# Performance work log

Hardware: AMD Instinct MI355X
Metric: run time of the kernel (lower is better)

Reference implementation:

```python
import jax, jax.numpy as jnp
import numpy as np

N_NODES = 100000

def gcn_conv(x, W, b, src, dst, norm, num_nodes):
    # Linear transform first (PyG GCNConv), then normalized scatter-add over edges.
    h = x @ W  # [N, d_out]
    msgs = norm[:, None] * h[src]  # gather source features, scale by sym norm
    out = jax.ops.segment_sum(msgs, dst, num_segments=num_nodes)
    return out + b

def gcn_norm(edge_index, num_nodes):
    # add self loops, compute deg^-1/2[src] * deg^-1/2[dst] per edge (PyG gcn_norm)
    loops = jnp.arange(num_nodes, dtype=edge_index.dtype)
    src = jnp.concatenate([edge_index[0], loops])
    dst = jnp.concatenate([edge_index[1], loops])
    deg = jax.ops.segment_sum(jnp.ones_like(dst, dtype=jnp.float32), dst, num_segments=num_nodes)
    dinv = jnp.where(deg > 0, jax.lax.rsqrt(deg), 0.0)
    norm = dinv[src] * dinv[dst]
    return src, dst, norm

def setup_inputs() -> dict:
    key = jax.random.key(0)
    k1, k2, k3, k4 = jax.random.split(key, 4)
    x = jax.random.normal(k1, (N_NODES, 512), dtype=jnp.float32)
    edge_index = jax.random.randint(k2, (2, 1600000), 0, N_NODES, dtype=jnp.int32)
    W1 = jax.random.normal(k3, (512, 128), dtype=jnp.float32) * (1.0 / np.sqrt(512))
    b1 = jnp.zeros((128,), dtype=jnp.float32)
    W2 = jax.random.normal(k4, (128, 40), dtype=jnp.float32) * (1.0 / np.sqrt(128))
    b2 = jnp.zeros((40,), dtype=jnp.float32)
    return {"x": x, "edge_index": edge_index, "W1": W1, "b1": b1, "W2": W2, "b2": b2}

def reference(x, edge_index, W1, b1, W2, b2):
    src, dst, norm = gcn_norm(edge_index, N_NODES)
    h = jax.nn.relu(gcn_conv(x, W1, b1, src, dst, norm, N_NODES))
    # dropout is identity in eval mode
    logits = gcn_conv(h, W2, b2, src, dst, norm, N_NODES)
    return jax.nn.log_softmax(logits, axis=1)
```

## Files before the change

### kernel.cpp

```cpp
#include <hip/hip_runtime.h>
#include <hip/hip_bf16.h>
#include <math.h>

typedef __attribute__((ext_vector_type(8))) short short8v;
typedef __attribute__((ext_vector_type(4))) unsigned short ushort4v;
typedef __attribute__((ext_vector_type(8))) unsigned short ushort8v;
typedef __attribute__((ext_vector_type(4))) unsigned uint4v;
typedef __attribute__((ext_vector_type(4))) float f32x4;

__device__ inline unsigned short f2bf(float f) {
    unsigned u = __float_as_uint(f);
    return (unsigned short)((u + 0x7fffu + ((u >> 16) & 1u)) >> 16);
}
__device__ inline float bflo(unsigned u) { return __uint_as_float(u << 16); }
__device__ inline float bfhi(unsigned u) { return __uint_as_float(u & 0xffff0000u); }
__device__ inline float bf1(unsigned short s) { return __uint_as_float((unsigned)s << 16); }
__device__ inline unsigned pk2(float a, float b) {
    __hip_bfloat162 h = __float22bfloat162_rn(make_float2(a, b));
    unsigned r;
    __builtin_memcpy(&r, &h, 4);
    return r;
}

__global__ void k_deg(const int* __restrict__ dst, int* __restrict__ deg,
                      int* __restrict__ rank, int E) {
    int e = blockIdx.x * blockDim.x + threadIdx.x;
    if (e < E) rank[e] = atomicAdd(&deg[dst[e]], 1);
}

__global__ __launch_bounds__(256) void k_bsum(const int* __restrict__ deg,
                                              int* __restrict__ bsum, int n) {
    __shared__ int r[256];
    int b = blockIdx.x, tid = threadIdx.x;
    int i0 = b * 1024 + tid * 4;
    int s = 0;
#pragma unroll
    for (int j = 0; j < 4; ++j)
        if (i0 + j < n) s += deg[i0 + j];
    r[tid] = s;
    __syncthreads();
    for (int off = 128; off > 0; off >>= 1) {
        if (tid < off) r[tid] += r[tid + off];
        __syncthreads();
    }
    if (tid == 0) bsum[b] = r[0];
}

__global__ __launch_bounds__(1024) void k_scan2(const int* __restrict__ bsum,
                                                int* __restrict__ bpre,
                                                int* __restrict__ total_out, int nb) {
    __shared__ int ls[1024];
    int tid = threadIdx.x;
    int v = (tid < nb) ? bsum[tid] : 0;
    ls[tid] = v;
    __syncthreads();
    for (int off = 1; off < 1024; off <<= 1) {
        int t = (tid >= off) ? ls[tid - off] : 0;
        __syncthreads();
        ls[tid] += t;
        __syncthreads();
    }
    if (tid < nb) bpre[tid] = ls[tid] - v;
    if (tid == 1023) *total_out = ls[1023];
}

__global__ __launch_bounds__(256) void k_scan3(const int* __restrict__ deg,
                                               const int* __restrict__ bpre,
                                               int* __restrict__ offsets,
                                               float* __restrict__ dinv, int n) {
    __shared__ int ts[256];
    int b = blockIdx.x, tid = threadIdx.x;
    int i0 = b * 1024 + tid * 4;
    int v[4] = {0, 0, 0, 0};
#pragma unroll
    for (int j = 0; j < 4; ++j)
        if (i0 + j < n) v[j] = deg[i0 + j];
    int s = v[0] + v[1] + v[2] + v[3];
    ts[tid] = s;
    __syncthreads();
    for (int off = 1; off < 256; off <<= 1) {
        int t = (tid >= off) ? ts[tid - off] : 0;
        __syncthreads();
        ts[tid] += t;
        __syncthreads();
    }
    int excl = bpre[b] + ts[tid] - s;
#pragma unroll
    for (int j = 0; j < 4; ++j) {
        if (i0 + j < n) {
            offsets[i0 + j] = excl;
            dinv[i0 + j] = rsqrtf((float)(v[j] + 1));
        }
        excl += v[j];
    }
}

__global__ void k_fill(const int* __restrict__ src, const int* __restrict__ dst,
                       const int* __restrict__ offsets, const int* __restrict__ rank,
                       int* __restrict__ esrc, int E) {
    int e = blockIdx.x * blockDim.x + threadIdx.x;
    if (e < E) esrc[offsets[dst[e]] + rank[e]] = src[e];
}

__global__ void k_wswz(const float* __restrict__ W1, unsigned short* __restrict__ Wswz) {
    int t = blockIdx.x * blockDim.x + threadIdx.x;
    if (t >= 16 * 8 * 64) return;
    int l = t & 63, cb = (t >> 6) & 7, ks = t >> 9;
    int col = cb * 16 + (l & 15);
    int kb = ks * 32 + 8 * (l >> 4);
    ushort8v w;
#pragma unroll
    for (int j = 0; j < 8; ++j) w[j] = f2bf(W1[(size_t)(kb + j) * 128 + col]);
    *(ushort8v*)(Wswz + (size_t)t * 8) = w;
}

#define AP 40
#define CP 132

__global__ __launch_bounds__(256) void k_gemm1(const float* __restrict__ x,
                                               const unsigned short* __restrict__ Wswz,
                                               const float* __restrict__ dinv,
                                               unsigned short* __restrict__ h0s, int M) {
    __shared__ __align__(16) unsigned short lds[64 * CP];
    int tid = threadIdx.x;
    int wc = tid >> 6, lane = tid & 63;
    int g = lane >> 4, lr = lane & 15;
    int brow = blockIdx.x * 64;

    int srow = tid >> 2, sq = tid & 3;
    int sgr = brow + srow;
    const float* xp = (sgr < M) ? (x + (size_t)sgr * 512 + sq * 8) : nullptr;

    f32x4 acc[4][2];
#pragma unroll
    for (int m = 0; m < 4; ++m)
#pragma unroll
        for (int n = 0; n < 2; ++n) acc[m][n] = (f32x4){0.f, 0.f, 0.f, 0.f};

    float4 paA = make_float4(0.f, 0.f, 0.f, 0.f), pbA = paA;
    float4 paB = paA, pbB = paA;
    if (xp) {
        paA = *(const float4*)xp;          pbA = *(const float4*)(xp + 4);
        paB = *(const float4*)(xp + 32);   pbB = *(const float4*)(xp + 36);
    }

#pragma unroll 1
    for (int ks = 0; ks < 16; ks += 2) {
        {
            unsigned short* As = lds;
            union { uint4v u; short8v s; } cv;
            cv.u[0] = pk2(paA.x, paA.y); cv.u[1] = pk2(paA.z, paA.w);
            cv.u[2] = pk2(pbA.x, pbA.y); cv.u[3] = pk2(pbA.z, pbA.w);
            *(short8v*)&As[srow * AP + sq * 8] = cv.s;
            __syncthreads();
            if (ks + 2 < 16 && xp) {
                const float* np = xp + (ks + 2) * 32;
                paA = *(const float4*)np; pbA = *(const float4*)(np + 4);
            }
            short8v bfr[2];
#pragma unroll
            for (int n = 0; n < 2; ++n) {
                int cb = wc * 2 + n;
                bfr[n] = *(const short8v*)(Wswz + (size_t)((ks * 8 + cb) * 64 + lane) * 8);
            }
            short8v afr[4];
#pragma unroll
            for (int m = 0; m < 4; ++m)
                afr[m] = *(const short8v*)&As[(m * 16 + lr) * AP + g * 8];
#pragma unroll
            for (int m = 0; m < 4; ++m)
#pragma unroll
                for (int n = 0; n < 2; ++n)
                    acc[m][n] = __builtin_amdgcn_mfma_f32_16x16x32_bf16(afr[m], bfr[n],
                                                                        acc[m][n], 0, 0, 0);
        }
        {
            unsigned short* As = lds + 2560;
            union { uint4v u; short8v s; } cv;
            cv.u[0] = pk2(paB.x, paB.y); cv.u[1] = pk2(paB.z, paB.w);
            cv.u[2] = pk2(pbB.x, pbB.y); cv.u[3] = pk2(pbB.z, pbB.w);
            *(short8v*)&As[srow * AP + sq * 8] = cv.s;
            __syncthreads();
            if (ks + 3 < 16 && xp) {
                const float* np = xp + (ks + 3) * 32;
                paB = *(const float4*)np; pbB = *(const float4*)(np + 4);
            }
            int k1 = ks + 1;
            short8v bfr[2];
#pragma unroll
            for (int n = 0; n < 2; ++n) {
                int cb = wc * 2 + n;
                bfr[n] = *(const short8v*)(Wswz + (size_t)((k1 * 8 + cb) * 64 + lane) * 8);
            }
            short8v afr[4];
#pragma unroll
            for (int m = 0; m < 4; ++m)
                afr[m] = *(const short8v*)&As[(m * 16 + lr) * AP + g * 8];
#pragma unroll
            for (int m = 0; m < 4; ++m)
#pragma unroll
                for (int n = 0; n < 2; ++n)
                    acc[m][n] = __builtin_amdgcn_mfma_f32_16x16x32_bf16(afr[m], bfr[n],
                                                                        acc[m][n], 0, 0, 0);
        }
    }
    __syncthreads();
#pragma unroll
    for (int m = 0; m < 4; ++m) {
        int row0 = m * 16 + g * 4;
        float dv[4];
#pragma unroll
        for (int r = 0; r < 4; ++r) {
            int gr = brow + row0 + r;
            dv[r] = (gr < M) ? dinv[gr] : 0.f;
        }
#pragma unroll
        for (int n = 0; n < 2; ++n) {
            int col = wc * 32 + n * 16 + lr;
#pragma unroll
            for (int r = 0; r < 4; ++r)
                lds[(row0 + r) * CP + col] = f2bf(acc[m][n][r] * dv[r]);
        }
    }
    __syncthreads();
    if (sgr < M) {
        unsigned short* dst = h0s + (size_t)sgr * 128;
        const unsigned short* src = &lds[srow * CP];
#pragma unroll
        for (int i = 0; i < 4; ++i) {
            int c = i * 32 + sq * 8;
            *(ushort4v*)(dst + c)     = *(const ushort4v*)(src + c);
            *(ushort4v*)(dst + c + 4) = *(const ushort4v*)(src + c + 4);
        }
    }
}

__global__ __launch_bounds__(256) void k_agg1(const unsigned short* __restrict__ h0s,
                                              const float* __restrict__ dinv,
                                              const int* __restrict__ offsets,
                                              const int* __restrict__ esrc,
                                              const float* __restrict__ b1,
                                              unsigned* __restrict__ h1b, int N) {
    int wid = (blockIdx.x * 256 + threadIdx.x) >> 6;
    if (wid >= N) return;
    int lane = threadIdx.x & 63;
    int half = lane >> 5, hl = lane & 31;
    const uint2* base = (const uint2*)h0s;
    uint2 us = base[(size_t)wid * 32 + hl];
    float ax0, ay0, ax1, ay1;
    if (half == 0) {
        ax0 = bflo(us.x); ay0 = bfhi(us.x); ax1 = bflo(us.y); ay1 = bfhi(us.y);
    } else {
        ax0 = ay0 = ax1 = ay1 = 0.f;
    }
    int beg = offsets[wid], end = offsets[wid + 1];
    for (int b0 = beg; b0 < end; b0 += 64) {
        int nb = min(64, end - b0);
        int idx = (lane < nb) ? esrc[b0 + lane] : 0;
        int k = 0;
        for (; k + 32 <= nb; k += 32) {
            uint2 v[16];
#pragma unroll
            for (int j = 0; j < 16; ++j) {
                int s = __shfl(idx, k + 2 * j + half);
                v[j] = base[(size_t)s * 32 + hl];
            }
#pragma unroll
            for (int j = 0; j < 16; ++j) {
                ax0 += bflo(v[j].x); ay0 += bfhi(v[j].x);
                ax1 += bflo(v[j].y); ay1 += bfhi(v[j].y);
            }
        }
        for (; k + 8 <= nb; k += 8) {
            uint2 v[4];
#pragma unroll
            for (int j = 0; j < 4; ++j) {
                int s = __shfl(idx, k + 2 * j + half);
                v[j] = base[(size_t)s * 32 + hl];
            }
#pragma unroll
            for (int j = 0; j < 4; ++j) {
                ax0 += bflo(v[j].x); ay0 += bfhi(v[j].x);
                ax1 += bflo(v[j].y); ay1 += bfhi(v[j].y);
            }
        }
        for (; k + 2 <= nb; k += 2) {
            int s = __shfl(idx, k + half);
            uint2 v = base[(size_t)s * 32 + hl];
            ax0 += bflo(v.x); ay0 += bfhi(v.x);
            ax1 += bflo(v.y); ay1 += bfhi(v.y);
        }
        if (k < nb) {
            int s = __shfl(idx, k);
            uint2 v = base[(size_t)s * 32 + hl];
            if (half == 0) {
                ax0 += bflo(v.x); ay0 += bfhi(v.x);
                ax1 += bflo(v.y); ay1 += bfhi(v.y);
            }
        }
    }
    ax0 += __shfl_xor(ax0, 32); ay0 += __shfl_xor(ay0, 32);
    ax1 += __shfl_xor(ax1, 32); ay1 += __shfl_xor(ay1, 32);
    if (half == 0) {
        float di = dinv[wid];
        float4 bb = ((const float4*)b1)[hl];
        float r0 = fmaxf(fmaf(di, ax0, bb.x), 0.f);
        float r1 = fmaxf(fmaf(di, ay0, bb.y), 0.f);
        float r2 = fmaxf(fmaf(di, ax1, bb.z), 0.f);
        float r3 = fmaxf(fmaf(di, ay1, bb.w), 0.f);
        uint2 o;
        o.x = pk2(r0, r1);
        o.y = pk2(r2, r3);
        ((uint2*)h1b)[(size_t)wid * 32 + hl] = o;
    }
}

__global__ __launch_bounds__(256) void k_gemm2(const unsigned* __restrict__ h1b,
                                               const float* __restrict__ W2,
                                               const float* __restrict__ dinv,
                                               unsigned short* __restrict__ h2s, int N) {
    __shared__ float w2s[128 * 40];
    int tid = threadIdx.x;
    for (int i = tid; i < 128 * 40; i += 256) w2s[i] = W2[i];
    __syncthreads();
    int r = blockIdx.x * 256 + tid;
    if (r >= N) return;
    const uint4v* row = (const uint4v*)(h1b + (size_t)r * 64);
    float acc[40];
#pragma unroll
    for (int c = 0; c < 40; ++c) acc[c] = 0.f;
    for (int c8 = 0; c8 < 16; ++c8) {
        uint4v u = row[c8];
        float aa[8];
#pragma unroll
        for (int j = 0; j < 4; ++j) {
            aa[2 * j]     = bflo(u[j]);
            aa[2 * j + 1] = bfhi(u[j]);
        }
        int kb = c8 * 8;
#pragma unroll
        for (int kk = 0; kk < 8; ++kk) {
            float av = aa[kk];
            const float4* wr = (const float4*)&w2s[(kb + kk) * 40];
#pragma unroll
            for (int c4 = 0; c4 < 10; ++c4) {
                float4 w = wr[c4];
                acc[c4 * 4 + 0] = fmaf(av, w.x, acc[c4 * 4 + 0]);
                acc[c4 * 4 + 1] = fmaf(av, w.y, acc[c4 * 4 + 1]);
                acc[c4 * 4 + 2] = fmaf(av, w.z, acc[c4 * 4 + 2]);
                acc[c4 * 4 + 3] = fmaf(av, w.w, acc[c4 * 4 + 3]);
            }
        }
    }
    float di = dinv[r];
    unsigned short* op = h2s + (size_t)r * 40;
#pragma unroll
    for (int c4 = 0; c4 < 10; ++c4) {
        ushort4v w;
        w[0] = f2bf(acc[c4 * 4 + 0] * di); w[1] = f2bf(acc[c4 * 4 + 1] * di);
        w[2] = f2bf(acc[c4 * 4 + 2] * di); w[3] = f2bf(acc[c4 * 4 + 3] * di);
        *(ushort4v*)(op + c4 * 4) = w;
    }
}

__global__ __launch_bounds__(256) void k_agg2(const unsigned short* __restrict__ h2s,
                                              const float* __restrict__ dinv,
                                              const int* __restrict__ offsets,
                                              const int* __restrict__ esrc,
                                              const float* __restrict__ b2,
                                              float* __restrict__ out, int N) {
    int wid = (blockIdx.x * 256 + threadIdx.x) >> 6;
    if (wid >= N) return;
    int lane = threadIdx.x & 63;
    int half = lane >> 5, hl = lane & 31;
    bool act = hl < 20;
    int cc = act ? hl : 0;
    const unsigned* base = (const unsigned*)h2s;
    unsigned us = base[(size_t)wid * 20 + cc];
    float a0 = 0.f, a1 = 0.f;
    if (half == 0 && act) { a0 = bflo(us); a1 = bfhi(us); }
    int beg = offsets[wid], end = offsets[wid + 1];
    for (int b0 = beg; b0 < end; b0 += 64) {
        int nb = min(64, end - b0);
        int idx = (lane < nb) ? esrc[b0 + lane] : 0;
        int k = 0;
        for (; k + 32 <= nb; k += 32) {
            unsigned v[16];
#pragma unroll
            for (int j = 0; j < 16; ++j) {
                int s = __shfl(idx, k + 2 * j + half);
                v[j] = base[(size_t)s * 20 + cc];
            }
#pragma unroll
            for (int j = 0; j < 16; ++j) { a0 += bflo(v[j]); a1 += bfhi(v[j]); }
        }
        for (; k + 8 <= nb; k += 8) {
            unsigned v[4];
#pragma unroll
            for (int j = 0; j < 4; ++j) {
                int s = __shfl(idx, k + 2 * j + half);
                v[j] = base[(size_t)s * 20 + cc];
            }
#pragma unroll
            for (int j = 0; j < 4; ++j) { a0 += bflo(v[j]); a1 += bfhi(v[j]); }
        }
        for (; k + 2 <= nb; k += 2) {
            int s = __shfl(idx, k + half);
            unsigned v = base[(size_t)s * 20 + cc];
            a0 += bflo(v); a1 += bfhi(v);
        }
        if (k < nb) {
            int s = __shfl(idx, k);
            unsigned v = base[(size_t)s * 20 + cc];
            if (half == 0) { a0 += bflo(v); a1 += bfhi(v); }
        }
    }
    a0 += __shfl_xor(a0, 32);
    a1 += __shfl_xor(a1, 32);
    float di = dinv[wid];
    float lx = 0.f, ly = 0.f;
    if (act) {
        float2 bp = ((const float2*)b2)[hl];
        lx = fmaf(di, a0, bp.x);
        ly = fmaf(di, a1, bp.y);
    }
    float m = act ? fmaxf(lx, ly) : -1e30f;
#pragma unroll
    for (int o = 32; o > 0; o >>= 1) m = fmaxf(m, __shfl_xor(m, o));
    float pv = act ? (__expf(lx - m) + __expf(ly - m)) : 0.f;
    float ssum = pv;
#pragma unroll
    for (int o = 32; o > 0; o >>= 1) ssum += __shfl_xor(ssum, o);
    ssum *= 0.5f;
    if (act && half == 0) {
        float lse = __logf(ssum);
        ((float2*)out)[(size_t)wid * 20 + hl] =
            make_float2(lx - m - lse, ly - m - lse);
    }
}

extern "C" void kernel_launch(void* const* d_in, const int* in_sizes, int n_in,
                              void* d_out, int out_size, void* d_ws, size_t ws_size,
                              hipStream_t stream) {
    const float* x  = (const float*)d_in[0];
    const int*   ei = (const int*)d_in[1];
    const float* W1 = (const float*)d_in[2];
    const float* b1 = (const float*)d_in[3];
    const float* W2 = (const float*)d_in[4];
    const float* b2 = (const float*)d_in[5];
    float* out = (float*)d_out;

    int N = in_sizes[0] / 512;
    int E = in_sizes[1] / 2;
    const int* esrc_in = ei;
    const int* edst_in = ei + E;
    int nb = (N + 1023) / 1024;

    char* p = (char*)d_ws;
    size_t off = 0;
    auto take = [&](size_t bytes) {
        size_t o = (off + 255) & ~(size_t)255;
        off = o + bytes;
        return (void*)(p + o);
    };
    unsigned short* h0s  = (unsigned short*)take((size_t)N * 128 * 2);
    unsigned*       h1b  = (unsigned*)take((size_t)N * 64 * 4);
    unsigned short* wswz = (unsigned short*)take((size_t)16 * 8 * 64 * 8 * 2);
    int*   deg  = (int*)take((size_t)N * 4);
    float* dinv = (float*)take((size_t)N * 4);
    int*   offs = (int*)take((size_t)(N + 1) * 4);
    int*   bsum = (int*)take((size_t)nb * 4);
    int*   bpre = (int*)take((size_t)nb * 4);
    int*   rank = (int*)take((size_t)E * 4);
    int*   esrc = (int*)take((size_t)E * 4);
    unsigned short* h2s = h0s;

    hipMemsetAsync(deg, 0, (size_t)N * 4, stream);

    k_wswz<<<32, 256, 0, stream>>>(W1, wswz);
    k_deg <<<(E + 255) / 256, 256, 0, stream>>>(edst_in, deg, rank, E);
    k_bsum <<<nb, 256, 0, stream>>>(deg, bsum, N);
    k_scan2<<<1, 1024, 0, stream>>>(bsum, bpre, offs + N, nb);
    k_scan3<<<nb, 256, 0, stream>>>(deg, bpre, offs, dinv, N);
    k_fill<<<(E + 255) / 256, 256, 0, stream>>>(esrc_in, edst_in, offs, rank, esrc, E);

    k_gemm1<<<(N + 63) / 64, 256, 0, stream>>>(x, wswz, dinv, h0s, N);
    k_agg1 <<<(N + 3) / 4, 256, 0, stream>>>(h0s, dinv, offs, esrc, b1, h1b, N);
    k_gemm2<<<(N + 255) / 256, 256, 0, stream>>>(h1b, W2, dinv, h2s, N);
    k_agg2 <<<(N + 3) / 4, 256, 0, stream>>>(h2s, dinv, offs, esrc, b2, out, N);
}
```

Measured before the change: 320.5 us.

## Merge independent kernels to overlap CSR fill with GEMM1 and W swizzle with degree count

Folds the W1 bf16 swizzle into the degree/atomic-rank kernel and the CSR edge fill into the first GEMM kernel, using block-index ranges to split work. This removes two kernel launches and lets the memory-bound scatter fill run concurrently with the compute-heavy GEMM. The fused GEMM kernel now declares its shared-memory buffer even for fill blocks, which may lower occupancy for those blocks and change scheduling.

```diff
diff --git a/kernel.cpp b/kernel.cpp
--- a/kernel.cpp
+++ b/kernel.cpp
@@ -22,10 +22,23 @@
     return r;
 }
 
-__global__ void k_deg(const int* __restrict__ dst, int* __restrict__ deg,
+__global__ void k_pre(const float* __restrict__ W1, unsigned short* __restrict__ Wswz,
+                      const int* __restrict__ dst, int* __restrict__ deg,
                       int* __restrict__ rank, int E) {
-    int e = blockIdx.x * blockDim.x + threadIdx.x;
-    if (e < E) rank[e] = atomicAdd(&deg[dst[e]], 1);
+    if (blockIdx.x < 32) {
+        int t = blockIdx.x * blockDim.x + threadIdx.x;
+        if (t >= 16 * 8 * 64) return;
+        int l = t & 63, cb = (t >> 6) & 7, ks = t >> 9;
+        int col = cb * 16 + (l & 15);
+        int kb = ks * 32 + 8 * (l >> 4);
+        ushort8v w;
+#pragma unroll
+        for (int j = 0; j < 8; ++j) w[j] = f2bf(W1[(size_t)(kb + j) * 128 + col]);
+        *(ushort8v*)(Wswz + (size_t)t * 8) = w;
+    } else {
+        int e = (blockIdx.x - 32) * blockDim.x + threadIdx.x;
+        if (e < E) rank[e] = atomicAdd(&deg[dst[e]], 1);
+    }
 }
 
 __global__ __launch_bounds__(256) void k_bsum(const int* __restrict__ deg,
@@ -95,33 +108,25 @@
     }
 }
 
-__global__ void k_fill(const int* __restrict__ src, const int* __restrict__ dst,
-                       const int* __restrict__ offsets, const int* __restrict__ rank,
-                       int* __restrict__ esrc, int E) {
-    int e = blockIdx.x * blockDim.x + threadIdx.x;
-    if (e < E) esrc[offsets[dst[e]] + rank[e]] = src[e];
-}
-
-__global__ void k_wswz(const float* __restrict__ W1, unsigned short* __restrict__ Wswz) {
-    int t = blockIdx.x * blockDim.x + threadIdx.x;
-    if (t >= 16 * 8 * 64) return;
-    int l = t & 63, cb = (t >> 6) & 7, ks = t >> 9;
-    int col = cb * 16 + (l & 15);
-    int kb = ks * 32 + 8 * (l >> 4);
-    ushort8v w;
-#pragma unroll
-    for (int j = 0; j < 8; ++j) w[j] = f2bf(W1[(size_t)(kb + j) * 128 + col]);
-    *(ushort8v*)(Wswz + (size_t)t * 8) = w;
-}
-
 #define AP 40
 #define CP 132
 
-__global__ __launch_bounds__(256) void k_gemm1(const float* __restrict__ x,
-                                               const unsigned short* __restrict__ Wswz,
-                                               const float* __restrict__ dinv,
-                                               unsigned short* __restrict__ h0s, int M) {
+__global__ __launch_bounds__(256) void k_fg(const float* __restrict__ x,
+                                            const unsigned short* __restrict__ Wswz,
+                                            const float* __restrict__ dinv,
+                                            unsigned short* __restrict__ h0s, int M,
+                                            const int* __restrict__ esrc_in,
+                                            const int* __restrict__ edst_in,
+                                            const int* __restrict__ offsets,
+                                            const int* __restrict__ rank,
+                                            int* __restrict__ esrc, int E) {
     __shared__ __align__(16) unsigned short lds[64 * CP];
+    int ngemm = (M + 63) >> 6;
+    if ((int)blockIdx.x >= ngemm) {
+        int e = ((int)blockIdx.x - ngemm) * 256 + (int)threadIdx.x;
+        if (e < E) esrc[offsets[edst_in[e]] + rank[e]] = esrc_in[e];
+        return;
+    }
     int tid = threadIdx.x;
     int wc = tid >> 6, lane = tid & 63;
     int g = lane >> 4, lr = lane & 15;
@@ -455,6 +460,8 @@
     const int* esrc_in = ei;
     const int* edst_in = ei + E;
     int nb = (N + 1023) / 1024;
+    int ngemm = (N + 63) / 64;
+    int nfill = (E + 255) / 256;
 
     char* p = (char*)d_ws;
     size_t off = 0;
@@ -477,14 +484,12 @@
 
     hipMemsetAsync(deg, 0, (size_t)N * 4, stream);
 
-    k_wswz<<<32, 256, 0, stream>>>(W1, wswz);
-    k_deg <<<(E + 255) / 256, 256, 0, stream>>>(edst_in, deg, rank, E);
+    k_pre  <<<32 + nfill, 256, 0, stream>>>(W1, wswz, edst_in, deg, rank, E);
     k_bsum <<<nb, 256, 0, stream>>>(deg, bsum, N);
     k_scan2<<<1, 1024, 0, stream>>>(bsum, bpre, offs + N, nb);
     k_scan3<<<nb, 256, 0, stream>>>(deg, bpre, offs, dinv, N);
-    k_fill<<<(E + 255) / 256, 256, 0, stream>>>(esrc_in, edst_in, offs, rank, esrc, E);
-
-    k_gemm1<<<(N + 63) / 64, 256, 0, stream>>>(x, wswz, dinv, h0s, N);
+    k_fg   <<<ngemm + nfill, 256, 0, stream>>>(x, wswz, dinv, h0s, N,
+                                               esrc_in, edst_in, offs, rank, esrc, E);
     k_agg1 <<<(N + 3) / 4, 256, 0, stream>>>(h0s, dinv, offs, esrc, b1, h1b, N);
     k_gemm2<<<(N + 255) / 256, 256, 0, stream>>>(h1b, W2, dinv, h2s, N);
     k_agg2 <<<(N + 3) / 4, 256, 0, stream>>>(h2s, dinv, offs, esrc, b2, out, N);
```

Result: faster. 307.5 us (-4.1%).
